# Performance work log

Hardware: AMD Instinct MI355X
Metric: run time of the kernel (lower is better)

Reference implementation:

```python
import jax, jax.numpy as jnp
import numpy as np

V, D, L = 32000, 1024, 2
B, S = 2, 1024
EPS = 1e-5


def _l2norm(x, eps=1e-6):
    return x * jax.lax.rsqrt(jnp.sum(x * x, axis=-1, keepdims=True) + eps)


def _rmsnorm(x, w, eps=1e-5):
    return x * jax.lax.rsqrt(jnp.mean(x * x, axis=-1, keepdims=True) + eps) * w


def _layernorm(x, g, b, eps=1e-5):
    mu = jnp.mean(x, axis=-1, keepdims=True)
    xc = x - mu
    var = jnp.mean(xc * xc, axis=-1, keepdims=True)
    return xc * jax.lax.rsqrt(var + eps) * g + b


def _delta_scan(q, k, v, beta):
    # q,k,v: [B,S,D]; beta: [B,S,1]. State S_t: [B,D,D] maps k->v.
    def step(St, inp):
        q_t, k_t, v_t, b_t = inp  # [B,D],[B,D],[B,D],[B,1]
        kS = jnp.einsum('bd,bde->be', k_t, St)
        St = St + jnp.einsum('bd,be->bde', k_t, b_t * (v_t - kS))
        o_t = jnp.einsum('bd,bde->be', q_t, St)
        return St, o_t

    xs = (q.swapaxes(0, 1), k.swapaxes(0, 1), v.swapaxes(0, 1), beta.swapaxes(0, 1))
    init = jnp.zeros((q.shape[0], q.shape[2], v.shape[2]), q.dtype)
    _, os = jax.lax.scan(step, init, xs)
    return os.swapaxes(0, 1)  # [B,S,D]


def setup_inputs() -> dict:
    key = jax.random.key(0)
    ks = jax.random.split(key, 10)
    sc = 0.02
    return {
        'tokens': jax.random.randint(ks[0], (B, S), 0, V, dtype=jnp.int32),
        'emb': jax.random.normal(ks[1], (V, D), jnp.float32) * sc,
        'Wq': jax.random.normal(ks[2], (L, D, D), jnp.float32) * sc,
        'Wk': jax.random.normal(ks[3], (L, D, D), jnp.float32) * sc,
        'Wv': jax.random.normal(ks[4], (L, D, D), jnp.float32) * sc,
        'Wb': jax.random.normal(ks[5], (L, D, 1), jnp.float32) * sc,
        'Wo': jax.random.normal(ks[6], (L, D, D), jnp.float32) * sc,
        'rms_w': jnp.ones((L, D), jnp.float32),
        'ln_g': jnp.ones((D,), jnp.float32),
        'ln_b': jnp.zeros((D,), jnp.float32),
        'head_w': jax.random.normal(ks[7], (D, V), jnp.float32) * sc,
    }


def reference(tokens, emb, Wq, Wk, Wv, Wb, Wo, rms_w, ln_g, ln_b, head_w):
    x = emb[tokens]  # [B,S,D]
    for l in range(L):
        q = _l2norm(jax.nn.silu(x @ Wq[l]))
        k = _l2norm(jax.nn.silu(x @ Wk[l]))
        v = jax.nn.silu(x @ Wv[l])
        beta = jax.nn.sigmoid(x @ Wb[l])  # [B,S,1]
        o = _delta_scan(q, k, v, beta)
        o = _rmsnorm(o, rms_w[l])
        x = o @ Wo[l]
    x = _layernorm(x, ln_g, ln_b, EPS)
    return x @ head_w  # [B,S,V]
```

## Files before the change

kernel.cpp:

```cpp
#include <hip/hip_runtime.h>
#include <hip/hip_bf16.h>


#define DD 1024
#define BB 2
#define SS 1024
#define LL 2
#define VV 32000

typedef __attribute__((ext_vector_type(8))) short bf16x8;
typedef __attribute__((ext_vector_type(4))) float f32x4;

__device__ __forceinline__ float sigmoidf_(float x) { return 1.0f / (1.0f + expf(-x)); }

__device__ __forceinline__ unsigned short f2bf(float f) {
    unsigned int u = __float_as_uint(f);
    u += 0x7fffu + ((u >> 16) & 1u);
    return (unsigned short)(u >> 16);
}

__global__ __launch_bounds__(256) void gather_rows(const int* __restrict__ tokens,
                                                   const float* __restrict__ emb,
                                                   float* __restrict__ x) {
    int row = blockIdx.x;
    int tok = tokens[row];
    const float4* src = (const float4*)(emb + (size_t)tok * DD);
    float4* dst = (float4*)(x + (size_t)row * DD);
    for (int i = threadIdx.x; i < DD / 4; i += 256) dst[i] = src[i];
}

template <int BM, int BN, int BK, int TM, int TN>
__global__ __launch_bounds__(256) void sgemm(const float* __restrict__ A,
                                             const float* __restrict__ B,
                                             float* __restrict__ C,
                                             int M, int N, int K) {
    constexpr int THREADS = (BM / TM) * (BN / TN);
    static_assert(THREADS == 256, "block must be 256");
    __shared__ float As[BK][BM + 4];
    __shared__ float Bs[BK][BN + 4];

    const int tid = threadIdx.x;
    const int tx = tid % (BN / TN);
    const int ty = tid / (BN / TN);
    const int row0 = blockIdx.y * BM;
    const int col0 = blockIdx.x * BN;

    float acc[TM][TN] = {};

    for (int k0 = 0; k0 < K; k0 += BK) {
        constexpr int A4 = BM * BK / 4;
        #pragma unroll
        for (int i = tid; i < A4; i += THREADS) {
            int r = i / (BK / 4);
            int q = i % (BK / 4);
            float4 f = *(const float4*)&A[(size_t)(row0 + r) * K + k0 + q * 4];
            As[q * 4 + 0][r] = f.x;
            As[q * 4 + 1][r] = f.y;
            As[q * 4 + 2][r] = f.z;
            As[q * 4 + 3][r] = f.w;
        }
        constexpr int B4 = BK * BN / 4;
        #pragma unroll
        for (int i = tid; i < B4; i += THREADS) {
            int r = i / (BN / 4);
            int q = i % (BN / 4);
            float4 f = *(const float4*)&B[(size_t)(k0 + r) * N + col0 + q * 4];
            *(float4*)&Bs[r][q * 4] = f;
        }
        __syncthreads();

        #pragma unroll
        for (int kr = 0; kr < BK; kr++) {
            float a[TM], b[TN];
            #pragma unroll
            for (int i = 0; i < TM; i += 4)
                *(float4*)&a[i] = *(const float4*)&As[kr][ty * TM + i];
            #pragma unroll
            for (int j = 0; j < TN; j += 4)
                *(float4*)&b[j] = *(const float4*)&Bs[kr][tx * TN + j];
            #pragma unroll
            for (int i = 0; i < TM; i++)
                #pragma unroll
                for (int j = 0; j < TN; j++)
                    acc[i][j] += a[i] * b[j];
        }
        __syncthreads();
    }

    #pragma unroll
    for (int i = 0; i < TM; i++)
        #pragma unroll
        for (int j = 0; j < TN; j += 4) {
            float4 f = {acc[i][j], acc[i][j + 1], acc[i][j + 2], acc[i][j + 3]};
            *(float4*)&C[(size_t)(row0 + ty * TM + i) * N + col0 + tx * TN + j] = f;
        }
}

__global__ __launch_bounds__(256) void gemm_bf16_tn(const unsigned short* __restrict__ A,
                                                    const unsigned short* __restrict__ Bt,
                                                    float* __restrict__ C,
                                                    int M, int N, int K) {
    __shared__ __align__(16) unsigned short As[128 * 32];
    __shared__ __align__(16) unsigned short Bs[128 * 32];

    const int tid = threadIdx.x;
    const int wave = tid >> 6;
    const int lane = tid & 63;
    const int row0 = blockIdx.y * 128;
    const int col0 = blockIdx.x * 128;
    const int wm = wave >> 1;
    const int wn = wave & 1;
    const int g = lane >> 4;
    const int fr = lane & 15;

    const int lr = lane >> 2;
    const int lk = (lane & 3) * 8;

    f32x4 acc[4][4] = {};

    for (int k0 = 0; k0 < K; k0 += 32) {
        __syncthreads();
        #pragma unroll
        for (int i = 0; i < 2; i++) {
            const int iss = wave * 2 + i;
            const unsigned short* ga = A + (size_t)(row0 + iss * 16 + lr) * K + k0 + lk;
            __builtin_amdgcn_global_load_lds(
                (const __attribute__((address_space(1))) void*)ga,
                (__attribute__((address_space(3))) void*)(As + iss * 512), 16, 0, 0);
            const unsigned short* gb = Bt + (size_t)(col0 + iss * 16 + lr) * K + k0 + lk;
            __builtin_amdgcn_global_load_lds(
                (const __attribute__((address_space(1))) void*)gb,
                (__attribute__((address_space(3))) void*)(Bs + iss * 512), 16, 0, 0);
        }
        __syncthreads();

        bf16x8 a[4], b[4];
        #pragma unroll
        for (int i = 0; i < 4; i++)
            a[i] = *(const bf16x8*)&As[(wm * 64 + i * 16 + fr) * 32 + g * 8];
        #pragma unroll
        for (int j = 0; j < 4; j++)
            b[j] = *(const bf16x8*)&Bs[(wn * 64 + j * 16 + fr) * 32 + g * 8];
        #pragma unroll
        for (int i = 0; i < 4; i++)
            #pragma unroll
            for (int j = 0; j < 4; j++)
                acc[i][j] = __builtin_amdgcn_mfma_f32_16x16x32_bf16(a[i], b[j], acc[i][j], 0, 0, 0);
    }

    #pragma unroll
    for (int i = 0; i < 4; i++) {
        const int rbase = row0 + wm * 64 + i * 16 + g * 4;
        #pragma unroll
        for (int j = 0; j < 4; j++) {
            const int c = col0 + wn * 64 + j * 16 + fr;
            #pragma unroll
            for (int ii = 0; ii < 4; ii++)
                C[(size_t)(rbase + ii) * N + c] = acc[i][j][ii];
        }
    }
}

__global__ __launch_bounds__(256) void f32_to_bf16_vec(const float* __restrict__ in,
                                                       unsigned short* __restrict__ out,
                                                       int n4) {
    int i = blockIdx.x * 256 + threadIdx.x;
    if (i < n4) {
        float4 f = ((const float4*)in)[i];
        ushort4 u = {f2bf(f.x), f2bf(f.y), f2bf(f.z), f2bf(f.w)};
        ((ushort4*)out)[i] = u;
    }
}

__global__ __launch_bounds__(256) void transpose_f32_bf16(const float* __restrict__ in,
                                                          unsigned short* __restrict__ out,
                                                          int K, int N) {
    __shared__ float tile[32][33];
    const int nb = blockIdx.x;
    const int kb = blockIdx.y;
    const int tx = threadIdx.x & 31;
    const int ty = threadIdx.x >> 5;
    #pragma unroll
    for (int i = 0; i < 32; i += 8)
        tile[ty + i][tx] = in[(size_t)(kb * 32 + ty + i) * N + nb * 32 + tx];
    __syncthreads();
    #pragma unroll
    for (int i = 0; i < 32; i += 8)
        out[(size_t)(nb * 32 + ty + i) * K + kb * 32 + tx] = f2bf(tile[tx][ty + i]);
}

__global__ __launch_bounds__(256) void silu_l2norm_kernel(float* __restrict__ buf) {
    __shared__ float tmp[4];
    size_t base = (size_t)blockIdx.x * DD;
    float vals[4];
    float ss = 0.0f;
    #pragma unroll
    for (int i = 0; i < 4; i++) {
        float xv = buf[base + threadIdx.x + i * 256];
        float s = xv * sigmoidf_(xv);
        vals[i] = s;
        ss += s * s;
    }
    #pragma unroll
    for (int off = 32; off; off >>= 1) ss += __shfl_xor(ss, off);
    if ((threadIdx.x & 63) == 0) tmp[threadIdx.x >> 6] = ss;
    __syncthreads();
    ss = tmp[0] + tmp[1] + tmp[2] + tmp[3];
    float sc = rsqrtf(ss + 1e-6f);
    #pragma unroll
    for (int i = 0; i < 4; i++) buf[base + threadIdx.x + i * 256] = vals[i] * sc;
}

__global__ __launch_bounds__(256) void silu_kernel(float* __restrict__ buf, int n) {
    int i = blockIdx.x * 256 + threadIdx.x;
    if (i < n) {
        float xv = buf[i];
        buf[i] = xv * sigmoidf_(xv);
    }
}

__global__ __launch_bounds__(256) void beta_kernel(const float* __restrict__ x,
                                                   const float* __restrict__ wb,
                                                   float* __restrict__ beta) {
    __shared__ float tmp[4];
    size_t base = (size_t)blockIdx.x * DD;
    float s = 0.0f;
    #pragma unroll
    for (int i = 0; i < 4; i++) {
        int idx = threadIdx.x + i * 256;
        s += x[base + idx] * wb[idx];
    }
    #pragma unroll
    for (int off = 32; off; off >>= 1) s += __shfl_xor(s, off);
    if ((threadIdx.x & 63) == 0) tmp[threadIdx.x >> 6] = s;
    __syncthreads();
    if (threadIdx.x == 0) beta[blockIdx.x] = sigmoidf_(tmp[0] + tmp[1] + tmp[2] + tmp[3]);
}

__global__ __launch_bounds__(256) void rmsnorm_kernel(float* __restrict__ buf,
                                                      const float* __restrict__ w) {
    __shared__ float tmp[4];
    size_t base = (size_t)blockIdx.x * DD;
    float vals[4];
    float ss = 0.0f;
    #pragma unroll
    for (int i = 0; i < 4; i++) {
        float xv = buf[base + threadIdx.x + i * 256];
        vals[i] = xv;
        ss += xv * xv;
    }
    #pragma unroll
    for (int off = 32; off; off >>= 1) ss += __shfl_xor(ss, off);
    if ((threadIdx.x & 63) == 0) tmp[threadIdx.x >> 6] = ss;
    __syncthreads();
    ss = tmp[0] + tmp[1] + tmp[2] + tmp[3];
    float sc = rsqrtf(ss * (1.0f / DD) + 1e-5f);
    #pragma unroll
    for (int i = 0; i < 4; i++) {
        int idx = threadIdx.x + i * 256;
        buf[base + idx] = vals[i] * sc * w[idx];
    }
}

__global__ __launch_bounds__(256) void layernorm_kernel(const float* __restrict__ in,
                                                        const float* __restrict__ g,
                                                        const float* __restrict__ b,
                                                        float* __restrict__ out) {
    __shared__ float tmp[4];
    size_t base = (size_t)blockIdx.x * DD;
    float vals[4];
    float s = 0.0f;
    #pragma unroll
    for (int i = 0; i < 4; i++) {
        float xv = in[base + threadIdx.x + i * 256];
        vals[i] = xv;
        s += xv;
    }
    #pragma unroll
    for (int off = 32; off; off >>= 1) s += __shfl_xor(s, off);
    if ((threadIdx.x & 63) == 0) tmp[threadIdx.x >> 6] = s;
    __syncthreads();
    float mu = (tmp[0] + tmp[1] + tmp[2] + tmp[3]) * (1.0f / DD);
    float vs = 0.0f;
    #pragma unroll
    for (int i = 0; i < 4; i++) {
        float c = vals[i] - mu;
        vals[i] = c;
        vs += c * c;
    }
    #pragma unroll
    for (int off = 32; off; off >>= 1) vs += __shfl_xor(vs, off);
    __syncthreads();
    if ((threadIdx.x & 63) == 0) tmp[threadIdx.x >> 6] = vs;
    __syncthreads();
    float var = (tmp[0] + tmp[1] + tmp[2] + tmp[3]) * (1.0f / DD);
    float sc = rsqrtf(var + 1e-5f);
    #pragma unroll
    for (int i = 0; i < 4; i++) {
        int idx = threadIdx.x + i * 256;
        out[base + idx] = vals[i] * sc * g[idx] + b[idx];
    }
}

__global__ __launch_bounds__(256) void delta_scan_kernel(const float* __restrict__ q,
                                                         const float* __restrict__ k,
                                                         const float* __restrict__ v,
                                                         const float* __restrict__ beta,
                                                         float* __restrict__ o) {
    __shared__ float lk[DD];
    __shared__ float lq[DD];
    const int nColBlk = DD / 4;
    const int batch = blockIdx.x / nColBlk;
    const int colBase = (blockIdx.x % nColBlk) * 4;
    const int w = threadIdx.x >> 6;
    const int lane = threadIdx.x & 63;
    const int col = colBase + w;
    const size_t base = (size_t)batch * SS * DD;

    float Sl[16];
    #pragma unroll
    for (int r = 0; r < 16; r++) Sl[r] = 0.0f;

    for (int t = 0; t < SS; t++) {
        const size_t rowoff = base + (size_t)t * DD;
        float4 fk = *(const float4*)&k[rowoff + threadIdx.x * 4];
        float4 fq = *(const float4*)&q[rowoff + threadIdx.x * 4];
        float bt = beta[batch * SS + t];
        float vt = v[rowoff + col];
        __syncthreads();
        *(float4*)&lk[threadIdx.x * 4] = fk;
        *(float4*)&lq[threadIdx.x * 4] = fq;
        __syncthreads();

        float kk[16], qq[16];
        #pragma unroll
        for (int r4 = 0; r4 < 4; r4++) {
            *(float4*)&kk[r4 * 4] = *(const float4*)&lk[lane * 16 + r4 * 4];
            *(float4*)&qq[r4 * 4] = *(const float4*)&lq[lane * 16 + r4 * 4];
        }

        float p = 0.0f;
        #pragma unroll
        for (int r = 0; r < 16; r++) p += kk[r] * Sl[r];
        #pragma unroll
        for (int off = 32; off; off >>= 1) p += __shfl_xor(p, off);

        float u = bt * (vt - p);

        float op = 0.0f;
        #pragma unroll
        for (int r = 0; r < 16; r++) {
            Sl[r] += kk[r] * u;
            op += qq[r] * Sl[r];
        }
        #pragma unroll
        for (int off = 32; off; off >>= 1) op += __shfl_xor(op, off);

        if (lane == 0) o[rowoff + col] = op;
    }
}

extern "C" void kernel_launch(void* const* d_in, const int* in_sizes, int n_in,
                              void* d_out, int out_size, void* d_ws, size_t ws_size,
                              hipStream_t stream) {
    const int* tokens   = (const int*)d_in[0];
    const float* emb    = (const float*)d_in[1];
    const float* Wq     = (const float*)d_in[2];
    const float* Wk     = (const float*)d_in[3];
    const float* Wv     = (const float*)d_in[4];
    const float* Wb     = (const float*)d_in[5];
    const float* Wo     = (const float*)d_in[6];
    const float* rms_w  = (const float*)d_in[7];
    const float* ln_g   = (const float*)d_in[8];
    const float* ln_b   = (const float*)d_in[9];
    const float* head_w = (const float*)d_in[10];
    float* out = (float*)d_out;

    const int M = BB * SS;
    const size_t ND = (size_t)M * DD;

    float* ws    = (float*)d_ws;
    float* x     = ws;
    float* qb    = ws + ND;
    float* kb    = ws + 2 * ND;
    float* vb    = ws + 3 * ND;
    float* ob    = ws + 4 * ND;
    float* xn    = ws + 5 * ND;
    float* betab = ws + 6 * ND;

    unsigned short* xnb = (unsigned short*)(ws + 6 * ND + M);
    unsigned short* hwb = xnb + (size_t)M * DD;
    const size_t need_bytes = (6 * ND + M) * sizeof(float) +
                              ((size_t)M * DD + (size_t)VV * DD) * sizeof(unsigned short);
    const bool bf16_head = (ws_size >= need_bytes);

    gather_rows<<<M, 256, 0, stream>>>(tokens, emb, x);

    for (int l = 0; l < LL; l++) {
        const float* wq = Wq + (size_t)l * DD * DD;
        const float* wk = Wk + (size_t)l * DD * DD;
        const float* wv = Wv + (size_t)l * DD * DD;
        const float* wb = Wb + (size_t)l * DD;
        const float* wo = Wo + (size_t)l * DD * DD;
        const float* rw = rms_w + (size_t)l * DD;

        dim3 g64(DD / 64, M / 64);
        sgemm<64, 64, 16, 4, 4><<<g64, 256, 0, stream>>>(x, wq, qb, M, DD, DD);
        silu_l2norm_kernel<<<M, 256, 0, stream>>>(qb);
        sgemm<64, 64, 16, 4, 4><<<g64, 256, 0, stream>>>(x, wk, kb, M, DD, DD);
        silu_l2norm_kernel<<<M, 256, 0, stream>>>(kb);
        sgemm<64, 64, 16, 4, 4><<<g64, 256, 0, stream>>>(x, wv, vb, M, DD, DD);
        silu_kernel<<<(M * DD + 255) / 256, 256, 0, stream>>>(vb, M * DD);
        beta_kernel<<<M, 256, 0, stream>>>(x, wb, betab);

        delta_scan_kernel<<<BB * (DD / 4), 256, 0, stream>>>(qb, kb, vb, betab, ob);

        rmsnorm_kernel<<<M, 256, 0, stream>>>(ob, rw);
        sgemm<64, 64, 16, 4, 4><<<g64, 256, 0, stream>>>(ob, wo, x, M, DD, DD);
    }

    layernorm_kernel<<<M, 256, 0, stream>>>(x, ln_g, ln_b, xn);

    if (bf16_head) {
        f32_to_bf16_vec<<<(M * DD / 4 + 255) / 256, 256, 0, stream>>>(xn, xnb, M * DD / 4);
        transpose_f32_bf16<<<dim3(VV / 32, DD / 32), 256, 0, stream>>>(head_w, hwb, DD, VV);
        gemm_bf16_tn<<<dim3(VV / 128, M / 128), 256, 0, stream>>>(xnb, hwb, out, M, VV, DD);
    } else {
        dim3 ghead(VV / 128, M / 128);
        sgemm<128, 128, 8, 8, 8><<<ghead, 256, 0, stream>>>(xn, head_w, out, M, VV, DD);
    }
}
```

Baseline: 3.555 ms.

## Double-buffer delta-scan k/q rows via direct global-to-LDS loads and fuse reductions

The sequential delta-scan loop now prefetches the next timestep's k and q rows straight into a second LDS buffer with global_load_lds, so global latency overlaps the current step's compute and one barrier per step is removed. The output is rewritten algebraically as q·S_old + (q·k)·u, which lets the three dot products (k·S, q·S, q·k) share one butterfly reduction chain instead of two dependent reductions. The LDS read pattern changes to match the direct-load layout. The risks are the reliance on vmcnt waits for correctness and slightly different float rounding.

```diff
diff --git a/kernel.cpp b/kernel.cpp
--- a/kernel.cpp
+++ b/kernel.cpp
@@ -307,54 +307,82 @@
                                                          const float* __restrict__ v,
                                                          const float* __restrict__ beta,
                                                          float* __restrict__ o) {
-    __shared__ float lk[DD];
-    __shared__ float lq[DD];
+    __shared__ __align__(16) float lk[2][DD];
+    __shared__ __align__(16) float lq[2][DD];
     const int nColBlk = DD / 4;
     const int batch = blockIdx.x / nColBlk;
     const int colBase = (blockIdx.x % nColBlk) * 4;
     const int w = threadIdx.x >> 6;
     const int lane = threadIdx.x & 63;
+    const int fr = lane & 15;
+    const int g = lane >> 4;
     const int col = colBase + w;
     const size_t base = (size_t)batch * SS * DD;
+    const int dbase = fr * 16 + g * 4;
+    const int stoff = w * 256 + lane * 4;
 
     float Sl[16];
     #pragma unroll
     for (int r = 0; r < 16; r++) Sl[r] = 0.0f;
 
+    {
+        const float* gk = k + base + stoff;
+        const float* gq = q + base + stoff;
+        __builtin_amdgcn_global_load_lds(
+            (const __attribute__((address_space(1))) void*)gk,
+            (__attribute__((address_space(3))) void*)(&lk[0][w * 256]), 16, 0, 0);
+        __builtin_amdgcn_global_load_lds(
+            (const __attribute__((address_space(1))) void*)gq,
+            (__attribute__((address_space(3))) void*)(&lq[0][w * 256]), 16, 0, 0);
+    }
+
     for (int t = 0; t < SS; t++) {
+        const int buf = t & 1;
         const size_t rowoff = base + (size_t)t * DD;
-        float4 fk = *(const float4*)&k[rowoff + threadIdx.x * 4];
-        float4 fq = *(const float4*)&q[rowoff + threadIdx.x * 4];
+
+        asm volatile("s_waitcnt vmcnt(0)" ::: "memory");
+        __builtin_amdgcn_s_barrier();
+
+        if (t + 1 < SS) {
+            const float* gk = k + rowoff + DD + stoff;
+            const float* gq = q + rowoff + DD + stoff;
+            __builtin_amdgcn_global_load_lds(
+                (const __attribute__((address_space(1))) void*)gk,
+                (__attribute__((address_space(3))) void*)(&lk[buf ^ 1][w * 256]), 16, 0, 0);
+            __builtin_amdgcn_global_load_lds(
+                (const __attribute__((address_space(1))) void*)gq,
+                (__attribute__((address_space(3))) void*)(&lq[buf ^ 1][w * 256]), 16, 0, 0);
+        }
+
         float bt = beta[batch * SS + t];
         float vt = v[rowoff + col];
-        __syncthreads();
-        *(float4*)&lk[threadIdx.x * 4] = fk;
-        *(float4*)&lq[threadIdx.x * 4] = fq;
-        __syncthreads();
 
         float kk[16], qq[16];
         #pragma unroll
         for (int r4 = 0; r4 < 4; r4++) {
-            *(float4*)&kk[r4 * 4] = *(const float4*)&lk[lane * 16 + r4 * 4];
-            *(float4*)&qq[r4 * 4] = *(const float4*)&lq[lane * 16 + r4 * 4];
-        }
-
-        float p = 0.0f;
-        #pragma unroll
-        for (int r = 0; r < 16; r++) p += kk[r] * Sl[r];
-        #pragma unroll
-        for (int off = 32; off; off >>= 1) p += __shfl_xor(p, off);
-
-        float u = bt * (vt - p);
-
-        float op = 0.0f;
+            *(float4*)&kk[r4 * 4] = *(const float4*)&lk[buf][r4 * 256 + dbase];
+            *(float4*)&qq[r4 * 4] = *(const float4*)&lq[buf][r4 * 256 + dbase];
+        }
+
+        float pk = 0.0f, pq = 0.0f, pqk = 0.0f;
         #pragma unroll
         for (int r = 0; r < 16; r++) {
-            Sl[r] += kk[r] * u;
-            op += qq[r] * Sl[r];
-        }
-        #pragma unroll
-        for (int off = 32; off; off >>= 1) op += __shfl_xor(op, off);
+            pk += kk[r] * Sl[r];
+            pq += qq[r] * Sl[r];
+            pqk += qq[r] * kk[r];
+        }
+        #pragma unroll
+        for (int off = 32; off; off >>= 1) {
+            pk += __shfl_xor(pk, off);
+            pq += __shfl_xor(pq, off);
+            pqk += __shfl_xor(pqk, off);
+        }
+
+        float u = bt * (vt - pk);
+        float op = pq + pqk * u;
+
+        #pragma unroll
+        for (int r = 0; r < 16; r++) Sl[r] += kk[r] * u;
 
         if (lane == 0) o[rowoff + col] = op;
     }
```

Result: slower. 3.900 ms (+9.7%).

## Rewrite delta scan as one wave per column with register prefetch

Applied to the files above, without the earlier changes.

The delta-rule scan now runs one 64-lane wave per output column instead of four waves sharing LDS-staged k/q. This removes the per-step __syncthreads and LDS round trip. The time loop is unrolled by two, so each step's k, q, beta and v loads are prefetched into registers while the previous step computes. The output is computed algebraically as q·S_old + (q·k)·u, which lets the three dot-product reductions run together and drops the second dependent shuffle chain. The cost is four times more global reads of k and q, one per wave instead of one per block, plus higher register use.

```diff
diff --git a/kernel.cpp b/kernel.cpp
--- a/kernel.cpp
+++ b/kernel.cpp
@@ -302,61 +302,84 @@
     }
 }
 
-__global__ __launch_bounds__(256) void delta_scan_kernel(const float* __restrict__ q,
-                                                         const float* __restrict__ k,
-                                                         const float* __restrict__ v,
-                                                         const float* __restrict__ beta,
-                                                         float* __restrict__ o) {
-    __shared__ float lk[DD];
-    __shared__ float lq[DD];
-    const int nColBlk = DD / 4;
-    const int batch = blockIdx.x / nColBlk;
-    const int colBase = (blockIdx.x % nColBlk) * 4;
-    const int w = threadIdx.x >> 6;
-    const int lane = threadIdx.x & 63;
-    const int col = colBase + w;
+#define DS_STEP(KK, QQ, BT, VT, ROWOFF)                                      \
+  {                                                                          \
+    float pk4[4], pq4[4], pqk4[4];                                           \
+    _Pragma("unroll") for (int r4 = 0; r4 < 4; r4++) {                       \
+      pk4[r4] = KK[r4 * 4] * Sl[r4 * 4];                                     \
+      pq4[r4] = QQ[r4 * 4] * Sl[r4 * 4];                                     \
+      pqk4[r4] = QQ[r4 * 4] * KK[r4 * 4];                                    \
+      _Pragma("unroll") for (int j = 1; j < 4; j++) {                        \
+        pk4[r4] += KK[r4 * 4 + j] * Sl[r4 * 4 + j];                          \
+        pq4[r4] += QQ[r4 * 4 + j] * Sl[r4 * 4 + j];                          \
+        pqk4[r4] += QQ[r4 * 4 + j] * KK[r4 * 4 + j];                         \
+      }                                                                      \
+    }                                                                        \
+    float pk = (pk4[0] + pk4[1]) + (pk4[2] + pk4[3]);                        \
+    float pq = (pq4[0] + pq4[1]) + (pq4[2] + pq4[3]);                        \
+    float pqk = (pqk4[0] + pqk4[1]) + (pqk4[2] + pqk4[3]);                   \
+    _Pragma("unroll") for (int off = 32; off; off >>= 1) {                   \
+      pk += __shfl_xor(pk, off);                                             \
+      pq += __shfl_xor(pq, off);                                             \
+      pqk += __shfl_xor(pqk, off);                                           \
+    }                                                                        \
+    float u = (BT) * ((VT)-pk);                                              \
+    float op = pq + pqk * u;                       \
+    _Pragma("unroll") for (int r = 0; r < 16; r++) Sl[r] += KK[r] * u;       \
+    if (lane == 0) o[(ROWOFF) + col] = op;                                   \
+  }
+
+__global__ __launch_bounds__(64) void delta_scan_kernel(const float* __restrict__ q,
+                                                        const float* __restrict__ k,
+                                                        const float* __restrict__ v,
+                                                        const float* __restrict__ beta,
+                                                        float* __restrict__ o) {
+    const int gid = blockIdx.x;
+    const int batch = gid >> 10;
+    const int col = gid & (DD - 1);
+    const int lane = threadIdx.x;
     const size_t base = (size_t)batch * SS * DD;
+    const int doff = lane * 4;
 
     float Sl[16];
     #pragma unroll
     for (int r = 0; r < 16; r++) Sl[r] = 0.0f;
 
-    for (int t = 0; t < SS; t++) {
-        const size_t rowoff = base + (size_t)t * DD;
-        float4 fk = *(const float4*)&k[rowoff + threadIdx.x * 4];
-        float4 fq = *(const float4*)&q[rowoff + threadIdx.x * 4];
-        float bt = beta[batch * SS + t];
-        float vt = v[rowoff + col];
-        __syncthreads();
-        *(float4*)&lk[threadIdx.x * 4] = fk;
-        *(float4*)&lq[threadIdx.x * 4] = fq;
-        __syncthreads();
-
-        float kk[16], qq[16];
+    float kA[16], qA[16], kB[16], qB[16];
+    float btA, vtA, btB, vtB;
+
+    #pragma unroll
+    for (int r4 = 0; r4 < 4; r4++) {
+        *(float4*)&kA[r4 * 4] = *(const float4*)&k[base + r4 * 256 + doff];
+        *(float4*)&qA[r4 * 4] = *(const float4*)&q[base + r4 * 256 + doff];
+    }
+    btA = beta[batch * SS];
+    vtA = v[base + col];
+
+    for (int t = 0; t < SS; t += 2) {
+        const size_t row0 = base + (size_t)t * DD;
+
         #pragma unroll
         for (int r4 = 0; r4 < 4; r4++) {
-            *(float4*)&kk[r4 * 4] = *(const float4*)&lk[lane * 16 + r4 * 4];
-            *(float4*)&qq[r4 * 4] = *(const float4*)&lq[lane * 16 + r4 * 4];
-        }
-
-        float p = 0.0f;
-        #pragma unroll
-        for (int r = 0; r < 16; r++) p += kk[r] * Sl[r];
-        #pragma unroll
-        for (int off = 32; off; off >>= 1) p += __shfl_xor(p, off);
-
-        float u = bt * (vt - p);
-
-        float op = 0.0f;
-        #pragma unroll
-        for (int r = 0; r < 16; r++) {
-            Sl[r] += kk[r] * u;
-            op += qq[r] * Sl[r];
-        }
-        #pragma unroll
-        for (int off = 32; off; off >>= 1) op += __shfl_xor(op, off);
-
-        if (lane == 0) o[rowoff + col] = op;
+            *(float4*)&kB[r4 * 4] = *(const float4*)&k[row0 + DD + r4 * 256 + doff];
+            *(float4*)&qB[r4 * 4] = *(const float4*)&q[row0 + DD + r4 * 256 + doff];
+        }
+        btB = beta[batch * SS + t + 1];
+        vtB = v[row0 + DD + col];
+
+        DS_STEP(kA, qA, btA, vtA, row0)
+
+        if (t + 2 < SS) {
+            #pragma unroll
+            for (int r4 = 0; r4 < 4; r4++) {
+                *(float4*)&kA[r4 * 4] = *(const float4*)&k[row0 + 2 * DD + r4 * 256 + doff];
+                *(float4*)&qA[r4 * 4] = *(const float4*)&q[row0 + 2 * DD + r4 * 256 + doff];
+            }
+            btA = beta[batch * SS + t + 2];
+            vtA = v[row0 + 2 * DD + col];
+        }
+
+        DS_STEP(kB, qB, btB, vtB, row0 + DD)
     }
 }
 
@@ -413,7 +436,7 @@
         silu_kernel<<<(M * DD + 255) / 256, 256, 0, stream>>>(vb, M * DD);
         beta_kernel<<<M, 256, 0, stream>>>(x, wb, betab);
 
-        delta_scan_kernel<<<BB * (DD / 4), 256, 0, stream>>>(qb, kb, vb, betab, ob);
+        delta_scan_kernel<<<BB * DD, 64, 0, stream>>>(qb, kb, vb, betab, ob);
 
         rmsnorm_kernel<<<M, 256, 0, stream>>>(ob, rw);
         sgemm<64, 64, 16, 4, 4><<<g64, 256, 0, stream>>>(ob, wo, x, M, DD, DD);
```

Result: faster. 3.251 ms (-8.6%).
